# Optimization experiments

Hardware: AMD Instinct MI355X
Metric: run time of the kernel (lower is better)

Reference implementation:

```python
import jax, jax.numpy as jnp
import numpy as np

F = 5            # n_feat = sum(feat_mask)
N_THETAS = 16
N_RHOS = 5
K = N_THETAS * N_RHOS   # 80 Gaussian kernel bins
R = 16           # n_rotations
MAX_RHO = 12.0
S = 1000         # n_samples (patches)
V = 200          # n_vertices per patch
EPS = 1e-5
TWO_PI = 2.0 * np.pi


def _initial_coords():
    # ConvLayer.compute_initial_coordinates: polar grid of (rho, theta) centers
    grid_rho = np.linspace(0.0, MAX_RHO, num=N_RHOS + 1)[1:]
    grid_theta = np.linspace(0.0, TWO_PI, num=N_THETAS + 1)[:-1]
    gr, gt = np.meshgrid(grid_rho, grid_theta)
    return gr.T.flatten().astype(np.float32), gt.T.flatten().astype(np.float32)


def setup_inputs() -> dict:
    key = jax.random.key(0)
    ks = jax.random.split(key, 5)
    feat = jax.random.normal(ks[0], (S, V, F), jnp.float32)
    rho = jax.random.uniform(ks[1], (S, V), jnp.float32) * MAX_RHO
    theta = jax.random.uniform(ks[2], (S, V), jnp.float32) * TWO_PI
    mask = (jax.random.uniform(ks[3], (S, V), jnp.float32) < 0.9).astype(jnp.float32)
    x = jnp.concatenate([feat, rho[..., None], theta[..., None], mask[..., None]], axis=-1)

    gr, gt = _initial_coords()
    mu_rho = jnp.tile(jnp.asarray(gr)[None, :], (F, 1))        # [F, K]
    mu_theta = jnp.tile(jnp.asarray(gt)[None, :], (F, 1))      # [F, K]
    sigma_rho = jnp.full((F, K), MAX_RHO / 8.0, jnp.float32)
    sigma_theta = jnp.ones((F, K), jnp.float32)
    # VarianceScaling(scale=1, fan_avg, uniform): limit = sqrt(3/fan_avg), fan_avg=K
    limit = float(np.sqrt(3.0 / K))
    W_conv = jax.random.uniform(ks[4], (F, K, K), jnp.float32, -limit, limit)
    b_conv = jnp.zeros((F, K), jnp.float32)
    return dict(x=x, mu_rho=mu_rho, sigma_rho=sigma_rho, mu_theta=mu_theta,
                sigma_theta=sigma_theta, W_conv=W_conv, b_conv=b_conv)


def reference(x, mu_rho, sigma_rho, mu_theta, sigma_theta, W_conv, b_conv):
    n_samples = x.shape[0]
    feat = jnp.moveaxis(x[..., :F], -1, 0)          # [F, S, V]
    rho = x[..., 5]                                 # [S, V]
    theta = x[..., 6]                               # [S, V]
    mask = x[..., 7]                                # [S, V]

    inv_sr = 1.0 / (jnp.square(sigma_rho) + EPS)    # [F, K]
    inv_st = 1.0 / (jnp.square(sigma_theta) + EPS)  # [F, K]
    # rho Gaussians are rotation-independent: [F, S, V, K]
    rho_g = jnp.exp(-jnp.square(rho[None, :, :, None] - mu_rho[:, None, None, :])
                    * inv_sr[:, None, None, :])

    def body(carry, k):
        th = jnp.mod(theta + k * (TWO_PI / R), TWO_PI)          # [S, V]
        th_g = jnp.exp(-jnp.square(th[None, :, :, None] - mu_theta[:, None, None, :])
                       * inv_st[:, None, None, :])              # [F, S, V, K]
        act = rho_g * th_g * mask[None, :, :, None]
        act = act / (jnp.sum(act, axis=-1, keepdims=True) + EPS)  # normalize over K bins
        desc = jnp.einsum('fsvk,fsv->fsk', act, feat)           # masked reduce over vertices
        cf = jnp.einsum('fsk,fkj->fsj', desc, W_conv) + b_conv[:, None, :]
        return jnp.maximum(carry, cf), None

    init = jnp.full((F, n_samples, K), -jnp.inf, x.dtype)
    conv, _ = jax.lax.scan(jax.checkpoint(body), init, jnp.arange(R, dtype=x.dtype))
    conv = jax.nn.relu(conv)                        # [F, S, K]
    # tf.stack(ret, axis=2) -> [S, K, F]; reshape [-1, K*F]
    return jnp.transpose(conv, (1, 2, 0)).reshape(n_samples, K * F)
```

## Files before the change

### kernel.cpp

```cpp
#include <hip/hip_runtime.h>
#include <math.h>

#define NS 1000
#define NV 200
#define NF 5
#define NK 80
#define EPSF 1e-5f

#define TWOPI_F 6.28318530717958647692f
#define STEP_F  0.39269908169872414f
#define INV_STEP_F 2.5464790894703254f

#define EH_OFF_H    7424
#define INV2_OFF    6288
#define INV2_STRIDE 225
#define MSRG_OFF    9888
#define SMEM_FLOATS 10088
#define G_STRIDE_H  232
#define DESC_STRIDE_H 488

typedef __attribute__((ext_vector_type(8))) short short8;
typedef __attribute__((ext_vector_type(4))) float f32x4;

static __device__ __forceinline__ float frcp(float v) {
    return __builtin_amdgcn_rcpf(v);
}
static __device__ __forceinline__ unsigned short f2bf(float x) {
    unsigned u = __float_as_uint(x);
    return (unsigned short)((u + 0x7FFFu + ((u >> 16) & 1u)) >> 16);
}

__global__ __launch_bounds__(512, 8) void lsres_fused(
        const float* __restrict__ x,
        const float* __restrict__ mu_rho,
        const float* __restrict__ sigma_rho,
        const float* __restrict__ mu_theta,
        const float* __restrict__ sigma_theta,
        const float* __restrict__ Wc,
        const float* __restrict__ bc,
        float* __restrict__ out) {
    __shared__ __align__(16) float smem[SMEM_FLOATS];
    unsigned short* smemh = (unsigned short*)smem;

    const int s   = blockIdx.x;
    const int tid = threadIdx.x;

    if (tid < NV) {
        const int v = tid;
        const float* xe = x + ((size_t)s * NV + v) * 8;
        float4 x0 = *(const float4*)(xe);
        float4 x1 = *(const float4*)(xe + 4);
        float rho = x1.y, theta = x1.z, mask = x1.w;
        float fm[5] = {x0.x * mask, x0.y * mask, x0.z * mask, x0.w * mask, x1.x * mask};
        float rg[5];
        float srg = 0.0f;
#pragma unroll
        for (int r = 0; r < 5; ++r) {
            float mr  = mu_rho[r * 16];
            float sr  = sigma_rho[r * 16];
            float isr = 1.0f / (sr * sr + EPSF);
            float d = rho - mr;
            rg[r] = __expf(-d * d * isr);
            srg += rg[r];
        }
#pragma unroll
        for (int f = 0; f < 5; ++f)
#pragma unroll
            for (int r = 0; r < 5; ++r)
                smemh[(f * 5 + r) * G_STRIDE_H + v] = f2bf(fm[f] * rg[r]);

        int m0 = (int)floorf(theta * INV_STEP_F + 0.5f) - 10;
        float sgt = sigma_theta[0];
        float ist = 1.0f / (sgt * sgt + EPSF);
        float m0d = (float)m0 * STEP_F;
#pragma unroll
        for (int cc = 0; cc < 21; ++cc) {
            float mu = fmaf((float)cc, STEP_F, m0d);
            float d  = theta - mu;
            smemh[EH_OFF_H + v * 23 + cc] = f2bf(__expf(-d * d * ist));
        }
        smem[MSRG_OFF + v] = mask * srg;
    } else if (tid < 224) {
        const int v = tid;
#pragma unroll
        for (int cc = 0; cc < 23; ++cc) smemh[EH_OFF_H + v * 23 + cc] = 0;
#pragma unroll
        for (int m = 0; m < 32; ++m) smemh[m * G_STRIDE_H + v] = 0;
    } else if (tid < 256) {
        for (int i = tid - 224; i < 7 * G_STRIDE_H; i += 32)
            smemh[25 * G_STRIDE_H + i] = 0;
    }
    __syncthreads();

#pragma unroll
    for (int p = 0; p < 8; ++p) {
        int idx = tid + p * 512;
        if (idx < 3600) {
            int v  = idx >> 4;
            int jj = idx & 15;
            unsigned bits;
            if (v < NV) {
                float theta = x[((size_t)s * NV + v) * 8 + 6];
                float msrg  = smem[MSRG_OFF + v];
                int   m0 = (int)floorf(theta * INV_STEP_F + 0.5f) - 10;
                float th = theta + (float)jj * STEP_F;
                int b = ((th >= TWOPI_F) ? 16 : 0) - jj - m0;
                float sT = 0.0f;
#pragma unroll
                for (int t = 0; t < 16; ++t) {
                    int ic = min(max(b + t, 0), 20);
                    sT += __uint_as_float((unsigned)smemh[EH_OFF_H + v * 23 + ic] << 16);
                }
                float inv = frcp(fmaf(msrg, sT, EPSF));
                bits = (__float_as_uint(inv) & 0xFFFFFF00u) | (unsigned)(b + 128);
            } else {
                bits = 128u;
            }
            smem[INV2_OFF + jj * INV2_STRIDE + v] = __uint_as_float(bits);
        }
    }
    __syncthreads();

    const int lane = tid & 63;
    const int wv   = tid >> 6;
    const int ln   = lane & 15;
    const int g    = lane >> 4;
    const int j0   = wv * 2, j1 = j0 + 1;

    f32x4 c00 = {0.f, 0.f, 0.f, 0.f};
    f32x4 c01 = {0.f, 0.f, 0.f, 0.f};
    f32x4 c10 = {0.f, 0.f, 0.f, 0.f};
    f32x4 c11 = {0.f, 0.f, 0.f, 0.f};
    const char* smemb = (const char*)smem;
    const int abase = ln * 464 + g * 16;

#pragma unroll 1
    for (int kb = 0; kb < 7; ++kb) {
        short8 a0 = *(const short8*)(smemb + abase + kb * 64);
        short8 a1 = *(const short8*)(smemb + abase + 7424 + kb * 64);
        const int vb = kb * 32 + g * 8;

        union Frag { unsigned u[4]; short8 v8; } B0, B1;
#define BUILD_B(DST, J)                                                              \
        {                                                                            \
            _Pragma("unroll")                                                        \
            for (int p = 0; p < 4; ++p) {                                            \
                float pb0 = smem[INV2_OFF + (J) * INV2_STRIDE + (vb + 2 * p)];       \
                float pb1 = smem[INV2_OFF + (J) * INV2_STRIDE + (vb + 2 * p + 1)];   \
                int ic0 = min(max(ln + (int)(__float_as_uint(pb0) & 255u) - 128, 0), 20); \
                int ic1 = min(max(ln + (int)(__float_as_uint(pb1) & 255u) - 128, 0), 20); \
                float e0 = __uint_as_float((unsigned)smemh[EH_OFF_H + (vb + 2 * p) * 23 + ic0] << 16); \
                float e1 = __uint_as_float((unsigned)smemh[EH_OFF_H + (vb + 2 * p + 1) * 23 + ic1] << 16); \
                float act0 = e0 * pb0;                                               \
                float act1 = e1 * pb1;                                               \
                asm("v_cvt_pk_bf16_f32 %0, %1, %2" : "=v"(DST.u[p]) : "v"(act0), "v"(act1)); \
            }                                                                        \
        }
        BUILD_B(B0, j0)
        BUILD_B(B1, j1)
#undef BUILD_B
        c00 = __builtin_amdgcn_mfma_f32_16x16x32_bf16(a0, B0.v8, c00, 0, 0, 0);
        c10 = __builtin_amdgcn_mfma_f32_16x16x32_bf16(a1, B0.v8, c10, 0, 0, 0);
        c01 = __builtin_amdgcn_mfma_f32_16x16x32_bf16(a0, B1.v8, c01, 0, 0, 0);
        c11 = __builtin_amdgcn_mfma_f32_16x16x32_bf16(a1, B1.v8, c11, 0, 0, 0);
    }
    __syncthreads();

    {
#pragma unroll
        for (int q = 0; q < 4; ++q) {
            int m = g * 4 + q;
            int f = (m * 13) >> 6;
            int r = m - 5 * f;
            int o = f * 96 + r * 16 + ln;
            unsigned pk;
            asm("v_cvt_pk_bf16_f32 %0, %1, %2" : "=v"(pk) : "v"(c00[q]), "v"(c01[q]));
            smemh[j0 * DESC_STRIDE_H + o] = (unsigned short)pk;
            smemh[j1 * DESC_STRIDE_H + o] = (unsigned short)(pk >> 16);
            int m2 = 16 + m;
            if (m2 < 25) {
                int f2 = (m2 * 13) >> 6;
                int r2 = m2 - 5 * f2;
                int o2 = f2 * 96 + r2 * 16 + ln;
                unsigned pk2;
                asm("v_cvt_pk_bf16_f32 %0, %1, %2" : "=v"(pk2) : "v"(c10[q]), "v"(c11[q]));
                smemh[j0 * DESC_STRIDE_H + o2] = (unsigned short)pk2;
                smemh[j1 * DESC_STRIDE_H + o2] = (unsigned short)(pk2 >> 16);
            }
        }
        unsigned* d32 = (unsigned*)smem;
        for (int i = tid; i < 640; i += 512) {
            int jj = i / 40;
            int rm = i - jj * 40;
            int ff = rm >> 3;
            int w  = rm & 7;
            d32[jj * 244 + ff * 48 + 40 + w] = 0;
        }
    }
    __syncthreads();

    for (int job = wv; job < 25; job += 8) {
        const int f  = job / 5;
        const int nt = job - f * 5;
        const float* Wf = Wc + f * (NK * NK) + nt * 16 + ln;

        f32x4 cc = {0.f, 0.f, 0.f, 0.f};
#pragma unroll
        for (int kb = 0; kb < 3; ++kb) {
            short8 afr = *(const short8*)((const char*)smem
                          + ln * 976 + (f * 96 + kb * 32 + g * 8) * 2);
            union { unsigned u[4]; short8 v8; } bfr;
#pragma unroll
            for (int p = 0; p < 4; ++p) {
                int k0 = kb * 32 + g * 8 + 2 * p;
                float w0 = Wf[min(k0, 79) * NK];
                float w1 = Wf[min(k0 + 1, 79) * NK];
                asm("v_cvt_pk_bf16_f32 %0, %1, %2" : "=v"(bfr.u[p]) : "v"(w0), "v"(w1));
            }
            cc = __builtin_amdgcn_mfma_f32_16x16x32_bf16(afr, bfr.v8, cc, 0, 0, 0);
        }
        float m = fmaxf(fmaxf(cc[0], cc[1]), fmaxf(cc[2], cc[3]));
        m = fmaxf(m, __shfl_xor(m, 16));
        m = fmaxf(m, __shfl_xor(m, 32));
        if (g == 0) {
            float val = fmaxf(m + bc[f * NK + nt * 16 + ln], 0.0f);
            out[(size_t)s * (NK * NF) + (nt * 16 + ln) * NF + f] = val;
        }
    }
}

extern "C" void kernel_launch(void* const* d_in, const int* in_sizes, int n_in,
                              void* d_out, int out_size, void* d_ws, size_t ws_size,
                              hipStream_t stream) {
    const float* x           = (const float*)d_in[0];
    const float* mu_rho      = (const float*)d_in[1];
    const float* sigma_rho   = (const float*)d_in[2];
    const float* mu_theta    = (const float*)d_in[3];
    const float* sigma_theta = (const float*)d_in[4];
    const float* Wc          = (const float*)d_in[5];
    const float* bc          = (const float*)d_in[6];
    float* out = (float*)d_out;

    lsres_fused<<<dim3(NS), dim3(512), 0, stream>>>(
        x, mu_rho, sigma_rho, mu_theta, sigma_theta, Wc, bc, out);
}
```

Before: 98.57 us.

## Use Gaussian recurrence and interpolated lookup table for theta normalization sums

```diff
diff --git a/kernel.cpp b/kernel.cpp
--- a/kernel.cpp
+++ b/kernel.cpp
@@ -10,12 +10,17 @@
 #define TWOPI_F 6.28318530717958647692f
 #define STEP_F  0.39269908169872414f
 #define INV_STEP_F 2.5464790894703254f
+#define STEP2_F 0.15421256876f
+#define FSCALE  40.743665431525205f
+#define FSTEP   0.02454369260617026f
 
 #define EH_OFF_H    7424
-#define INV2_OFF    6288
+#define E_STRIDE_H  21
+#define INV2_OFF    6064
 #define INV2_STRIDE 225
-#define MSRG_OFF    9888
-#define SMEM_FLOATS 10088
+#define MSRG_OFF    9664
+#define F_OFF       9864
+#define SMEM_FLOATS 10121
 #define G_STRIDE_H  232
 #define DESC_STRIDE_H 488
 
@@ -26,8 +31,9 @@
     return __builtin_amdgcn_rcpf(v);
 }
 static __device__ __forceinline__ unsigned short f2bf(float x) {
-    unsigned u = __float_as_uint(x);
-    return (unsigned short)((u + 0x7FFFu + ((u >> 16) & 1u)) >> 16);
+    unsigned r;
+    asm("v_cvt_pk_bf16_f32 %0, %1, %2" : "=v"(r) : "v"(x), "v"(x));
+    return (unsigned short)r;
 }
 
 __global__ __launch_bounds__(512, 8) void lsres_fused(
@@ -72,23 +78,43 @@
         int m0 = (int)floorf(theta * INV_STEP_F + 0.5f) - 10;
         float sgt = sigma_theta[0];
         float ist = 1.0f / (sgt * sgt + EPSF);
-        float m0d = (float)m0 * STEP_F;
-#pragma unroll
-        for (int cc = 0; cc < 21; ++cc) {
-            float mu = fmaf((float)cc, STEP_F, m0d);
-            float d  = theta - mu;
-            smemh[EH_OFF_H + v * 23 + cc] = f2bf(__expf(-d * d * ist));
-        }
+        float u  = theta - (float)(m0 + 10) * STEP_F;
+        float Ec = __expf(-u * u * ist);
+        float Ru = __expf((2.0f * u * STEP_F - STEP2_F) * ist);
+        float Kc = __expf(-2.0f * STEP2_F * ist);
+        float Rd = Kc * frcp(Ru);
+        unsigned short* eRow = smemh + EH_OFF_H + v * E_STRIDE_H;
+        eRow[10] = f2bf(Ec);
+        float e = Ec, r = Ru;
+#pragma unroll
+        for (int q = 11; q <= 20; ++q) { e *= r; eRow[q] = f2bf(e); r *= Kc; }
+        e = Ec; r = Rd;
+#pragma unroll
+        for (int q = 9; q >= 0; --q)  { e *= r; eRow[q] = f2bf(e); r *= Kc; }
         smem[MSRG_OFF + v] = mask * srg;
     } else if (tid < 224) {
         const int v = tid;
 #pragma unroll
-        for (int cc = 0; cc < 23; ++cc) smemh[EH_OFF_H + v * 23 + cc] = 0;
+        for (int cc = 0; cc < E_STRIDE_H; ++cc) smemh[EH_OFF_H + v * E_STRIDE_H + cc] = 0;
 #pragma unroll
         for (int m = 0; m < 32; ++m) smemh[m * G_STRIDE_H + v] = 0;
     } else if (tid < 256) {
         for (int i = tid - 224; i < 7 * G_STRIDE_H; i += 32)
             smemh[25 * G_STRIDE_H + i] = 0;
+    } else {
+        const int ft = tid - 256;
+        float sgt = sigma_theta[0];
+        float ist = 1.0f / (sgt * sgt + EPSF);
+        float Kc  = __expf(-2.0f * STEP2_F * ist);
+        for (int en = ft; en < 257; en += 256) {
+            float xx   = (float)en * FSTEP;
+            float term = __expf(-xx * xx * ist);
+            float r    = __expf((2.0f * xx * STEP_F - STEP2_F) * ist);
+            float Fv   = term;
+#pragma unroll
+            for (int t = 1; t < 16; ++t) { term *= r; Fv += term; r *= Kc; }
+            smem[F_OFF + en] = Fv;
+        }
     }
     __syncthreads();
 
@@ -104,13 +130,15 @@
                 float msrg  = smem[MSRG_OFF + v];
                 int   m0 = (int)floorf(theta * INV_STEP_F + 0.5f) - 10;
                 float th = theta + (float)jj * STEP_F;
-                int b = ((th >= TWOPI_F) ? 16 : 0) - jj - m0;
-                float sT = 0.0f;
-#pragma unroll
-                for (int t = 0; t < 16; ++t) {
-                    int ic = min(max(b + t, 0), 20);
-                    sT += __uint_as_float((unsigned)smemh[EH_OFF_H + v * 23 + ic] << 16);
-                }
+                int   w  = (th >= TWOPI_F);
+                int   b  = (w ? 16 : 0) - jj - m0;
+                float thp = w ? (th - TWOPI_F) : th;
+                float pos = thp * FSCALE;
+                int   i   = min((int)pos, 255);
+                float fr  = pos - (float)i;
+                float Flo = smem[F_OFF + i];
+                float Fhi = smem[F_OFF + i + 1];
+                float sT  = fmaf(fr, Fhi - Flo, Flo);
                 float inv = frcp(fmaf(msrg, sT, EPSF));
                 bits = (__float_as_uint(inv) & 0xFFFFFF00u) | (unsigned)(b + 128);
             } else {
@@ -149,8 +177,8 @@
                 float pb1 = smem[INV2_OFF + (J) * INV2_STRIDE + (vb + 2 * p + 1)];   \
                 int ic0 = min(max(ln + (int)(__float_as_uint(pb0) & 255u) - 128, 0), 20); \
                 int ic1 = min(max(ln + (int)(__float_as_uint(pb1) & 255u) - 128, 0), 20); \
-                float e0 = __uint_as_float((unsigned)smemh[EH_OFF_H + (vb + 2 * p) * 23 + ic0] << 16); \
-                float e1 = __uint_as_float((unsigned)smemh[EH_OFF_H + (vb + 2 * p + 1) * 23 + ic1] << 16); \
+                float e0 = __uint_as_float((unsigned)smemh[EH_OFF_H + (vb + 2 * p) * E_STRIDE_H + ic0] << 16); \
+                float e1 = __uint_as_float((unsigned)smemh[EH_OFF_H + (vb + 2 * p + 1) * E_STRIDE_H + ic1] << 16); \
                 float act0 = e0 * pb0;                                               \
                 float act1 = e1 * pb1;                                               \
                 asm("v_cvt_pk_bf16_f32 %0, %1, %2" : "=v"(DST.u[p]) : "v"(act0), "v"(act1)); \
```

Result: faster. 92.62 us (-6.0%).
